# Optimization experiments

Hardware: AMD Instinct MI355X
Metric: run time of the kernel (lower is better)

The kernel has to match this reference:

```python
import jax, jax.numpy as jnp
import numpy as np

NUM_HEADS = 16
D_MODEL = 1024
HEAD_DIM = D_MODEL // NUM_HEADS
SCALE = 8.0 / HEAD_DIM  # use_mup=True
LN_EPS = 1e-5


def setup_inputs() -> dict:
    key = jax.random.key(0)
    ks = jax.random.split(key, 8)
    B, N, M = 2, 2048, 2048
    std = 1.0 / np.sqrt(D_MODEL)
    return {
        "x1": jax.random.normal(ks[0], (B, N, D_MODEL), jnp.float32),
        "x2": jax.random.normal(ks[1], (B, M, D_MODEL), jnp.float32),
        "Wq": jax.random.normal(ks[2], (D_MODEL, D_MODEL), jnp.float32) * std,
        "Wk": jax.random.normal(ks[3], (D_MODEL, D_MODEL), jnp.float32) * std,
        "Wv": jax.random.normal(ks[4], (D_MODEL, D_MODEL), jnp.float32) * std,
        "Wp": jax.random.normal(ks[5], (D_MODEL, D_MODEL), jnp.float32) * std,
        "bp": jnp.zeros((D_MODEL,), jnp.float32),
        "ln_g": jnp.ones((HEAD_DIM,), jnp.float32),
        "ln_b": jnp.zeros((HEAD_DIM,), jnp.float32),
    }


def _layernorm(x, g, b):
    # LayerNorm over last dim (head_dim), eps=1e-5, biased variance (torch default)
    mu = jnp.mean(x, axis=-1, keepdims=True)
    var = jnp.mean(jnp.square(x - mu), axis=-1, keepdims=True)
    return (x - mu) * jax.lax.rsqrt(var + LN_EPS) * g + b


def reference(x1, x2, Wq, Wk, Wv, Wp, bp, ln_g, ln_b):
    B, N, C = x1.shape
    M = x2.shape[1]
    H, D = NUM_HEADS, HEAD_DIM
    # torch Linear: y = x @ W.T  (no qkv bias); reshape to [B, H, L, D]
    q = (x1 @ Wq.T).reshape(B, N, H, D).transpose(0, 2, 1, 3)
    k = (x2 @ Wk.T).reshape(B, M, H, D).transpose(0, 2, 1, 3)
    v = (x2 @ Wv.T).reshape(B, M, H, D).transpose(0, 2, 1, 3)
    # per-head QK LayerNorm (shared params)
    q = _layernorm(q, ln_g, ln_b)
    k = _layernorm(k, ln_g, ln_b)
    q = q * SCALE
    attn = jnp.einsum("bhnd,bhmd->bhnm", q, k)
    attn = jax.nn.softmax(attn, axis=-1)  # causal=False, attn_drop=0
    out = jnp.einsum("bhnm,bhmd->bhnd", attn, v)
    out = out.transpose(0, 2, 1, 3).reshape(B, N, C)
    return out @ Wp.T + bp
```

## Files before the change

### kernel.cpp

```cpp
#include <hip/hip_runtime.h>

#define DEV static __device__ __forceinline__

using bf16x8 = __attribute__((ext_vector_type(8))) short;
using f32x4  = __attribute__((ext_vector_type(4))) float;
using f32x16 = __attribute__((ext_vector_type(16))) float;

#if __has_builtin(__builtin_amdgcn_exp2f)
#define EXP2(x) __builtin_amdgcn_exp2f(x)
#else
#define EXP2(x) exp2f(x)
#endif

DEV unsigned short f2bf(float f) {
  union { float f; unsigned u; } v; v.f = f;
  return (unsigned short)((v.u + 0x7fffu + ((v.u >> 16) & 1u)) >> 16);
}
DEV unsigned pk2(float lo, float hi) {
  return (unsigned)f2bf(lo) | ((unsigned)f2bf(hi) << 16);
}
DEV unsigned cvtpk(float lo, float hi) {
  unsigned r;
  asm("v_cvt_pk_bf16_f32 %0, %1, %2" : "=v"(r) : "v"(lo), "v"(hi));
  return r;
}
DEV void pl32swap(unsigned &a, unsigned &b) {
  asm("v_permlane32_swap_b32 %0, %1" : "+v"(a), "+v"(b));
}
DEV bf16x8 mk8(unsigned a, unsigned b, unsigned c, unsigned d) {
  union { unsigned u[4]; bf16x8 v; } t;
  t.u[0] = a; t.u[1] = b; t.u[2] = c; t.u[3] = d;
  return t.v;
}
DEV f32x4 mfma16(bf16x8 a, bf16x8 b, f32x4 c) {
  return __builtin_amdgcn_mfma_f32_16x16x32_bf16(a, b, c, 0, 0, 0);
}
DEV f32x16 mfma32(bf16x8 a, bf16x8 b, f32x16 c) {
  return __builtin_amdgcn_mfma_f32_32x32x16_bf16(a, b, c, 0, 0, 0);
}
DEV f32x16 zero16() {
  f32x16 z;
#pragma unroll
  for (int i = 0; i < 16; ++i) z[i] = 0.f;
  return z;
}

typedef const __attribute__((address_space(1))) unsigned int* gas1;
typedef __attribute__((address_space(3))) unsigned int* las3;
DEV void gl16(const void* g, void* l) {
  __builtin_amdgcn_global_load_lds((gas1)g, (las3)l, 16, 0, 0);
}

__global__ __launch_bounds__(256, 8)
void conv_bf16(const float* __restrict__ x1, const float* __restrict__ x2,
               const float* __restrict__ Wq, const float* __restrict__ Wk,
               const float* __restrict__ Wv, const float* __restrict__ Wp,
               unsigned short* __restrict__ o)
{
  size_t e = ((size_t)blockIdx.x * 256 + threadIdx.x) * 8;
  const float* s; size_t off;
  if (e < 4194304u)       { s = x1; off = e; }
  else if (e < 8388608u)  { s = x2; off = e - 4194304u; }
  else if (e < 9437184u)  { s = Wq; off = e - 8388608u; }
  else if (e < 10485760u) { s = Wk; off = e - 9437184u; }
  else if (e < 11534336u) { s = Wv; off = e - 10485760u; }
  else                    { s = Wp; off = e - 11534336u; }
  const float4* p = reinterpret_cast<const float4*>(s + off);
  float4 a = p[0], b = p[1];
  int4 r;
  r.x = (int)cvtpk(a.x, a.y); r.y = (int)cvtpk(a.z, a.w);
  r.z = (int)cvtpk(b.x, b.y); r.w = (int)cvtpk(b.z, b.w);
  *reinterpret_cast<int4*>(o + e) = r;
}

__global__ __launch_bounds__(256, 2)
void gemm_qkv_bf(const unsigned short* __restrict__ xb,
                 const float* __restrict__ lg, const float* __restrict__ lb,
                 unsigned short* __restrict__ qb, unsigned short* __restrict__ kb,
                 unsigned short* __restrict__ vtb)
{
  __shared__ short As[128 * 64];
  __shared__ short Bs[128 * 64];
  const int tid = threadIdx.x;
  const int l = tid & 63, w = tid >> 6;
  const int wr = w >> 1, wc = w & 1;
  const int z = blockIdx.z;
  const unsigned short* A = (z == 0) ? xb : (xb + 4194304);
  const unsigned short* W = xb + 8388608 + (size_t)z * 1048576;
  const int id = blockIdx.x + (blockIdx.y << 3);
  const int tl = ((id & 7) << 5) | (id >> 3);
  const int bx = tl & 7, by = tl >> 3;
  const int brow = by * 128, bcol = bx * 128;

  const f32x4 zero = {0.f, 0.f, 0.f, 0.f};
  f32x4 acc[4][4];
#pragma unroll
  for (int mi = 0; mi < 4; ++mi)
#pragma unroll
    for (int ni = 0; ni < 4; ++ni) acc[mi][ni] = zero;

  const int srow = w * 32 + (l >> 3);
  const int scol = (l & 7) * 8;

  for (int kt = 0; kt < 16; ++kt) {
    const unsigned short* ga = A + (size_t)(brow + srow) * 1024 + kt * 64 + scol;
    const unsigned short* gb = W + (size_t)(bcol + srow) * 1024 + kt * 64 + scol;
#pragma unroll
    for (int i = 0; i < 4; ++i) {
      gl16(ga + (size_t)i * 8 * 1024, &As[(w * 32 + i * 8) * 64]);
      gl16(gb + (size_t)i * 8 * 1024, &Bs[(w * 32 + i * 8) * 64]);
    }
    __syncthreads();
#pragma unroll
    for (int kk = 0; kk < 2; ++kk) {
      const int k0 = kk * 32 + ((l >> 4) << 3);
      bf16x8 af[4], bfr[4];
#pragma unroll
      for (int mi = 0; mi < 4; ++mi)
        af[mi] = *reinterpret_cast<const bf16x8*>(
            &As[((wr << 6) + (mi << 4) + (l & 15)) * 64 + k0]);
#pragma unroll
      for (int ni = 0; ni < 4; ++ni)
        bfr[ni] = *reinterpret_cast<const bf16x8*>(
            &Bs[((wc << 6) + (ni << 4) + (l & 15)) * 64 + k0]);
#pragma unroll
      for (int mi = 0; mi < 4; ++mi)
#pragma unroll
        for (int ni = 0; ni < 4; ++ni)
          acc[mi][ni] = mfma16(af[mi], bfr[ni], acc[mi][ni]);
    }
    __syncthreads();
  }

  if (z < 2) {
    unsigned short* dst = (z == 0) ? qb : kb;
    const float scl = (z == 0) ? 0.18033688011112042f : 1.0f;
    const int h = bx * 2 + wc;
    float gw4[4], bw4[4];
#pragma unroll
    for (int ni = 0; ni < 4; ++ni) {
      gw4[ni] = lg[ni * 16 + (l & 15)] * scl;
      bw4[ni] = lb[ni * 16 + (l & 15)] * scl;
    }
#pragma unroll
    for (int mi = 0; mi < 4; ++mi) {
      float ylo[4];
#pragma unroll
      for (int r = 0; r < 4; ++r) {
        float v0 = acc[mi][0][r], v1 = acc[mi][1][r];
        float v2 = acc[mi][2][r], v3 = acc[mi][3][r];
        float s  = (v0 + v1) + (v2 + v3);
        float s2 = (v0 * v0 + v1 * v1) + (v2 * v2 + v3 * v3);
#pragma unroll
        for (int off = 1; off < 16; off <<= 1) {
          s  += __shfl_xor(s, off);
          s2 += __shfl_xor(s2, off);
        }
        float mean = s * (1.f / 64.f);
        float var  = s2 * (1.f / 64.f) - mean * mean;
        float rstd = rsqrtf(var + 1e-5f);
        float y[4];
        y[0] = (v0 - mean) * rstd * gw4[0] + bw4[0];
        y[1] = (v1 - mean) * rstd * gw4[1] + bw4[1];
        y[2] = (v2 - mean) * rstd * gw4[2] + bw4[2];
        y[3] = (v3 - mean) * rstd * gw4[3] + bw4[3];
        if (!(r & 1)) {
          ylo[0] = y[0]; ylo[1] = y[1]; ylo[2] = y[2]; ylo[3] = y[3];
        } else {
          int rowg0 = brow + (wr << 6) + (mi << 4) + ((l >> 4) << 2) + r - 1;
          int b = rowg0 >> 11, n = rowg0 & 2047;
          unsigned short* base =
              dst + (((size_t)(b * 16 + h) << 11) + n) * 64 + (l & 15);
#pragma unroll
          for (int ni = 0; ni < 4; ++ni) {
            unsigned u = cvtpk(ylo[ni], y[ni]);
            base[ni * 16]      = (unsigned short)(u & 0xffffu);
            base[ni * 16 + 64] = (unsigned short)(u >> 16);
          }
        }
      }
    }
  } else {
    const int bb = brow >> 11;
    const int nblk = brow & 2047;
#pragma unroll
    for (int mi = 0; mi < 4; ++mi)
#pragma unroll
      for (int ni = 0; ni < 4; ++ni) {
        int n0 = nblk + (wr << 6) + (mi << 4) + ((l >> 4) << 2);
        int colg = bcol + (wc << 6) + (ni << 4) + (l & 15);
        int h = colg >> 6, d = colg & 63;
        unsigned u0 = cvtpk(acc[mi][ni][0], acc[mi][ni][1]);
        unsigned u1 = cvtpk(acc[mi][ni][2], acc[mi][ni][3]);
        int2 u; u.x = (int)u0; u.y = (int)u1;
        *reinterpret_cast<int2*>(
            &vtb[((size_t)(bb * 16 + h) * 64 + d) * 2048 + n0]) = u;
      }
  }
}

__global__ __launch_bounds__(128)
void attn_fwd(const unsigned short* __restrict__ Q,
              const unsigned short* __restrict__ K,
              const unsigned short* __restrict__ Vt,
              unsigned short* __restrict__ O)
{
  __shared__ short Ks[2][64 * 64];
  __shared__ short Vs[2][64 * 64];
  const int tid = threadIdx.x, w = tid >> 6, l = tid & 63;
  const int lo5 = l & 31, hi = l >> 5;
  const int bh = blockIdx.y;
  const int qbase = blockIdx.x * 64 + w * 32;
  const unsigned short* Qg = Q + ((size_t)bh * 2048 + qbase) * 64;
  const unsigned short* Kg = K + (size_t)bh * 2048 * 64;
  const unsigned short* Vg = Vt + (size_t)bh * 64 * 2048;

  bf16x8 qf[4];
#pragma unroll
  for (int ks = 0; ks < 4; ++ks)
    qf[ks] = *reinterpret_cast<const bf16x8*>(Qg + lo5 * 64 + ks * 16 + hi * 8);

  f32x16 oc0 = zero16(), oc1 = zero16();
  float lsum = 0.f;

  const int srow = tid >> 3;
  const int sc8 = (tid & 7) * 8;
  const int swz = sc8 ^ ((srow & 7) << 3);

  int4 ka0, ka1, ka2, ka3, va0, va1, va2, va3;
  ka0 = *reinterpret_cast<const int4*>(Kg + (srow)      * 64 + sc8);
  ka1 = *reinterpret_cast<const int4*>(Kg + (srow + 16) * 64 + sc8);
  ka2 = *reinterpret_cast<const int4*>(Kg + (srow + 32) * 64 + sc8);
  ka3 = *reinterpret_cast<const int4*>(Kg + (srow + 48) * 64 + sc8);
  va0 = *reinterpret_cast<const int4*>(Vg + (size_t)(srow)      * 2048 + sc8);
  va1 = *reinterpret_cast<const int4*>(Vg + (size_t)(srow + 16) * 2048 + sc8);
  va2 = *reinterpret_cast<const int4*>(Vg + (size_t)(srow + 32) * 2048 + sc8);
  va3 = *reinterpret_cast<const int4*>(Vg + (size_t)(srow + 48) * 2048 + sc8);
  *reinterpret_cast<int4*>(&Ks[0][((srow)      << 6) + swz]) = ka0;
  *reinterpret_cast<int4*>(&Ks[0][((srow + 16) << 6) + swz]) = ka1;
  *reinterpret_cast<int4*>(&Ks[0][((srow + 32) << 6) + swz]) = ka2;
  *reinterpret_cast<int4*>(&Ks[0][((srow + 48) << 6) + swz]) = ka3;
  *reinterpret_cast<int4*>(&Vs[0][((srow)      << 6) + swz]) = va0;
  *reinterpret_cast<int4*>(&Vs[0][((srow + 16) << 6) + swz]) = va1;
  *reinterpret_cast<int4*>(&Vs[0][((srow + 32) << 6) + swz]) = va2;
  *reinterpret_cast<int4*>(&Vs[0][((srow + 48) << 6) + swz]) = va3;
  __syncthreads();

  const unsigned short* kp = Kg + 4096 + srow * 64 + sc8;
  const unsigned short* vp = Vg + 64 + (size_t)srow * 2048 + sc8;

  for (int it = 0; it < 32; ++it) {
    const int cur = it & 1;
    const short* Kc = Ks[cur];
    const short* Vc = Vs[cur];

    if (it < 31) {
      ka0 = *reinterpret_cast<const int4*>(kp);
      ka1 = *reinterpret_cast<const int4*>(kp + 1024);
      ka2 = *reinterpret_cast<const int4*>(kp + 2048);
      ka3 = *reinterpret_cast<const int4*>(kp + 3072);
      va0 = *reinterpret_cast<const int4*>(vp);
      va1 = *reinterpret_cast<const int4*>(vp + 32768);
      va2 = *reinterpret_cast<const int4*>(vp + 65536);
      va3 = *reinterpret_cast<const int4*>(vp + 98304);
      kp += 4096; vp += 64;
    }

    f32x16 s0 = zero16(), s1 = zero16();
    __builtin_amdgcn_s_setprio(1);
#pragma unroll
    for (int ks = 0; ks < 4; ++ks) {
      const int colc = (16 * ks + 8 * hi) ^ ((lo5 & 7) << 3);
      bf16x8 k0 = *reinterpret_cast<const bf16x8*>(&Kc[(lo5 << 6) + colc]);
      s0 = mfma32(k0, qf[ks], s0);
      bf16x8 k1 = *reinterpret_cast<const bf16x8*>(&Kc[((32 + lo5) << 6) + colc]);
      s1 = mfma32(k1, qf[ks], s1);
    }
    __builtin_amdgcn_s_setprio(0);

    auto pvsub = [&](const f32x16& sv, int jbase) {
      float p0[16];
#pragma unroll
      for (int r = 0; r < 16; ++r) p0[r] = EXP2(sv[r]);
      lsum += (((p0[0] + p0[1]) + (p0[2] + p0[3])) +
               ((p0[4] + p0[5]) + (p0[6] + p0[7]))) +
              (((p0[8] + p0[9]) + (p0[10] + p0[11])) +
               ((p0[12] + p0[13]) + (p0[14] + p0[15])));
#pragma unroll
      for (int f = 0; f < 2; ++f) {
        unsigned x  = cvtpk(p0[8 * f + 0], p0[8 * f + 1]);
        unsigned zz = cvtpk(p0[8 * f + 2], p0[8 * f + 3]);
        unsigned y  = cvtpk(p0[8 * f + 4], p0[8 * f + 5]);
        unsigned ww = cvtpk(p0[8 * f + 6], p0[8 * f + 7]);
        pl32swap(x, y);
        pl32swap(zz, ww);
        bf16x8 pa = mk8(x, zz, y, ww);
        const int colc = (jbase + 16 * f + 8 * hi);
        bf16x8 v0 = *reinterpret_cast<const bf16x8*>(
            &Vc[(lo5 << 6) + (colc ^ ((lo5 & 7) << 3))]);
        bf16x8 v1 = *reinterpret_cast<const bf16x8*>(
            &Vc[((32 + lo5) << 6) + (colc ^ ((lo5 & 7) << 3))]);
        __builtin_amdgcn_s_setprio(1);
        oc0 = mfma32(pa, v0, oc0);
        oc1 = mfma32(pa, v1, oc1);
        __builtin_amdgcn_s_setprio(0);
      }
    };
    pvsub(s0, 0);
    pvsub(s1, 32);

    if (it < 31) {
      const int nb = cur ^ 1;
      *reinterpret_cast<int4*>(&Ks[nb][((srow)      << 6) + swz]) = ka0;
      *reinterpret_cast<int4*>(&Ks[nb][((srow + 16) << 6) + swz]) = ka1;
      *reinterpret_cast<int4*>(&Ks[nb][((srow + 32) << 6) + swz]) = ka2;
      *reinterpret_cast<int4*>(&Ks[nb][((srow + 48) << 6) + swz]) = ka3;
      *reinterpret_cast<int4*>(&Vs[nb][((srow)      << 6) + swz]) = va0;
      *reinterpret_cast<int4*>(&Vs[nb][((srow + 16) << 6) + swz]) = va1;
      *reinterpret_cast<int4*>(&Vs[nb][((srow + 32) << 6) + swz]) = va2;
      *reinterpret_cast<int4*>(&Vs[nb][((srow + 48) << 6) + swz]) = va3;
    }
    __syncthreads();
  }

  lsum += __shfl_xor(lsum, 32);
  float inv = 1.f / lsum;
  unsigned short* Og = O + ((size_t)(bh >> 4) * 2048 + qbase) * 1024 + (bh & 15) * 64;
#pragma unroll
  for (int r = 0; r < 16; ++r) {
    int qrow = (r & 3) + 8 * (r >> 2) + 4 * hi;
    float ir = __shfl(inv, qrow);
    Og[qrow * 1024 + lo5]      = f2bf(oc0[r] * ir);
    Og[qrow * 1024 + 32 + lo5] = f2bf(oc1[r] * ir);
  }
}

__global__ __launch_bounds__(256, 2)
void gemm_out_bf(const unsigned short* __restrict__ ob,
                 const unsigned short* __restrict__ wpb,
                 const float* __restrict__ bp, float* __restrict__ out)
{
  __shared__ short As[128 * 64];
  __shared__ short Bs[128 * 64];
  const int tid = threadIdx.x;
  const int l = tid & 63, w = tid >> 6;
  const int wr = w >> 1, wc = w & 1;
  const int id = blockIdx.x + (blockIdx.y << 3);
  const int tl = ((id & 7) << 5) | (id >> 3);
  const int brow = (tl >> 3) * 128, bcol = (tl & 7) * 128;

  const f32x4 zero = {0.f, 0.f, 0.f, 0.f};
  f32x4 acc[4][4];
#pragma unroll
  for (int mi = 0; mi < 4; ++mi)
#pragma unroll
    for (int ni = 0; ni < 4; ++ni) acc[mi][ni] = zero;

  const int srow = w * 32 + (l >> 3);
  const int scol = (l & 7) * 8;

  for (int kt = 0; kt < 16; ++kt) {
    const unsigned short* ga = ob + (size_t)(brow + srow) * 1024 + kt * 64 + scol;
    const unsigned short* gb = wpb + (size_t)(bcol + srow) * 1024 + kt * 64 + scol;
#pragma unroll
    for (int i = 0; i < 4; ++i) {
      gl16(ga + (size_t)i * 8 * 1024, &As[(w * 32 + i * 8) * 64]);
      gl16(gb + (size_t)i * 8 * 1024, &Bs[(w * 32 + i * 8) * 64]);
    }
    __syncthreads();
#pragma unroll
    for (int kk = 0; kk < 2; ++kk) {
      const int k0 = kk * 32 + ((l >> 4) << 3);
      bf16x8 af[4], bfr[4];
#pragma unroll
      for (int mi = 0; mi < 4; ++mi)
        af[mi] = *reinterpret_cast<const bf16x8*>(
            &As[((wr << 6) + (mi << 4) + (l & 15)) * 64 + k0]);
#pragma unroll
      for (int ni = 0; ni < 4; ++ni)
        bfr[ni] = *reinterpret_cast<const bf16x8*>(
            &Bs[((wc << 6) + (ni << 4) + (l & 15)) * 64 + k0]);
#pragma unroll
      for (int mi = 0; mi < 4; ++mi)
#pragma unroll
        for (int ni = 0; ni < 4; ++ni)
          acc[mi][ni] = mfma16(af[mi], bfr[ni], acc[mi][ni]);
    }
    __syncthreads();
  }

  float bias[4];
#pragma unroll
  for (int ni = 0; ni < 4; ++ni)
    bias[ni] = bp[bcol + (wc << 6) + (ni << 4) + (l & 15)];
#pragma unroll
  for (int mi = 0; mi < 4; ++mi)
#pragma unroll
    for (int ni = 0; ni < 4; ++ni)
#pragma unroll
      for (int r = 0; r < 4; ++r) {
        int rowg = brow + (wr << 6) + (mi << 4) + ((l >> 4) << 2) + r;
        int colg = bcol + (wc << 6) + (ni << 4) + (l & 15);
        out[(size_t)rowg * 1024 + colg] = acc[mi][ni][r] + bias[ni];
      }
}

extern "C" void kernel_launch(void* const* d_in, const int* in_sizes, int n_in,
                              void* d_out, int out_size, void* d_ws, size_t ws_size,
                              hipStream_t stream)
{
  const float* x1 = (const float*)d_in[0];
  const float* x2 = (const float*)d_in[1];
  const float* Wq = (const float*)d_in[2];
  const float* Wk = (const float*)d_in[3];
  const float* Wv = (const float*)d_in[4];
  const float* Wp = (const float*)d_in[5];
  const float* bp = (const float*)d_in[6];
  const float* lg = (const float*)d_in[7];
  const float* lb = (const float*)d_in[8];

  char* wsb = (char*)d_ws;
  unsigned short* xb   = (unsigned short*)wsb;
  unsigned short* qb   = (unsigned short*)(wsb + 25165824);
  unsigned short* kb   = qb + 4194304;
  unsigned short* vtb  = kb + 4194304;
  unsigned short* obuf = vtb + 4194304;
  float* out = (float*)d_out;

  conv_bf16<<<6144, 256, 0, stream>>>(x1, x2, Wq, Wk, Wv, Wp, xb);
  gemm_qkv_bf<<<dim3(8, 32, 3), 256, 0, stream>>>(xb, lg, lb, qb, kb, vtb);
  attn_fwd<<<dim3(32, 32), 128, 0, stream>>>(qb, kb, vtb, obuf);
  gemm_out_bf<<<dim3(8, 32), 256, 0, stream>>>(obuf,
      xb + 11534336, bp, out);
}
```

Baseline: 130.3 us.

## Split attention over key range into two halves and combine partials

Splits the attention kernel's key loop into two halves via a third grid dimension, doubling the number of blocks. Each half writes unnormalized bf16 partial outputs and row sums to workspace, and a new combine kernel adds them and normalizes. The row-sum accumulation moves from scalar adds to an extra MFMA against a ones vector. This aims to improve occupancy and load balance on the GPU, at the cost of an extra launch, extra global traffic, and bf16 rounding of the partials.

Result: slower. 143.1 us (+9.8%).

```diff
diff --git a/kernel.cpp b/kernel.cpp
--- a/kernel.cpp
+++ b/kernel.cpp
@@ -16,8 +16,9 @@
   union { float f; unsigned u; } v; v.f = f;
   return (unsigned short)((v.u + 0x7fffu + ((v.u >> 16) & 1u)) >> 16);
 }
-DEV unsigned pk2(float lo, float hi) {
-  return (unsigned)f2bf(lo) | ((unsigned)f2bf(hi) << 16);
+DEV float bf2f(unsigned short b) {
+  union { unsigned u; float f; } v; v.u = ((unsigned)b) << 16;
+  return v.f;
 }
 DEV unsigned cvtpk(float lo, float hi) {
   unsigned r;
@@ -203,13 +204,16 @@
 void attn_fwd(const unsigned short* __restrict__ Q,
               const unsigned short* __restrict__ K,
               const unsigned short* __restrict__ Vt,
-              unsigned short* __restrict__ O)
+              unsigned short* __restrict__ pnum,
+              float* __restrict__ plsum)
 {
   __shared__ short Ks[2][64 * 64];
   __shared__ short Vs[2][64 * 64];
   const int tid = threadIdx.x, w = tid >> 6, l = tid & 63;
   const int lo5 = l & 31, hi = l >> 5;
   const int bh = blockIdx.y;
+  const int half = blockIdx.z;
+  const int tbase = half * 16;
   const int qbase = blockIdx.x * 64 + w * 32;
   const unsigned short* Qg = Q + ((size_t)bh * 2048 + qbase) * 64;
   const unsigned short* Kg = K + (size_t)bh * 2048 * 64;
@@ -219,23 +223,27 @@
 #pragma unroll
   for (int ks = 0; ks < 4; ++ks)
     qf[ks] = *reinterpret_cast<const bf16x8*>(Qg + lo5 * 64 + ks * 16 + hi * 8);
-
-  f32x16 oc0 = zero16(), oc1 = zero16();
-  float lsum = 0.f;
+  const bf16x8 ones = mk8(0x3F803F80u, 0x3F803F80u, 0x3F803F80u, 0x3F803F80u);
+
+  f32x16 oc0 = zero16(), oc1 = zero16(), ls = zero16();
 
   const int srow = tid >> 3;
   const int sc8 = (tid & 7) * 8;
   const int swz = sc8 ^ ((srow & 7) << 3);
 
   int4 ka0, ka1, ka2, ka3, va0, va1, va2, va3;
-  ka0 = *reinterpret_cast<const int4*>(Kg + (srow)      * 64 + sc8);
-  ka1 = *reinterpret_cast<const int4*>(Kg + (srow + 16) * 64 + sc8);
-  ka2 = *reinterpret_cast<const int4*>(Kg + (srow + 32) * 64 + sc8);
-  ka3 = *reinterpret_cast<const int4*>(Kg + (srow + 48) * 64 + sc8);
-  va0 = *reinterpret_cast<const int4*>(Vg + (size_t)(srow)      * 2048 + sc8);
-  va1 = *reinterpret_cast<const int4*>(Vg + (size_t)(srow + 16) * 2048 + sc8);
-  va2 = *reinterpret_cast<const int4*>(Vg + (size_t)(srow + 32) * 2048 + sc8);
-  va3 = *reinterpret_cast<const int4*>(Vg + (size_t)(srow + 48) * 2048 + sc8);
+  {
+    const unsigned short* k0g = Kg + tbase * 4096;
+    const unsigned short* v0g = Vg + tbase * 64;
+    ka0 = *reinterpret_cast<const int4*>(k0g + (srow)      * 64 + sc8);
+    ka1 = *reinterpret_cast<const int4*>(k0g + (srow + 16) * 64 + sc8);
+    ka2 = *reinterpret_cast<const int4*>(k0g + (srow + 32) * 64 + sc8);
+    ka3 = *reinterpret_cast<const int4*>(k0g + (srow + 48) * 64 + sc8);
+    va0 = *reinterpret_cast<const int4*>(v0g + (size_t)(srow)      * 2048 + sc8);
+    va1 = *reinterpret_cast<const int4*>(v0g + (size_t)(srow + 16) * 2048 + sc8);
+    va2 = *reinterpret_cast<const int4*>(v0g + (size_t)(srow + 32) * 2048 + sc8);
+    va3 = *reinterpret_cast<const int4*>(v0g + (size_t)(srow + 48) * 2048 + sc8);
+  }
   *reinterpret_cast<int4*>(&Ks[0][((srow)      << 6) + swz]) = ka0;
   *reinterpret_cast<int4*>(&Ks[0][((srow + 16) << 6) + swz]) = ka1;
   *reinterpret_cast<int4*>(&Ks[0][((srow + 32) << 6) + swz]) = ka2;
@@ -246,15 +254,15 @@
   *reinterpret_cast<int4*>(&Vs[0][((srow + 48) << 6) + swz]) = va3;
   __syncthreads();
 
-  const unsigned short* kp = Kg + 4096 + srow * 64 + sc8;
-  const unsigned short* vp = Vg + 64 + (size_t)srow * 2048 + sc8;
-
-  for (int it = 0; it < 32; ++it) {
+  const unsigned short* kp = Kg + (tbase + 1) * 4096 + srow * 64 + sc8;
+  const unsigned short* vp = Vg + (tbase + 1) * 64 + (size_t)srow * 2048 + sc8;
+
+  for (int it = 0; it < 16; ++it) {
     const int cur = it & 1;
     const short* Kc = Ks[cur];
     const short* Vc = Vs[cur];
 
-    if (it < 31) {
+    if (it < 15) {
       ka0 = *reinterpret_cast<const int4*>(kp);
       ka1 = *reinterpret_cast<const int4*>(kp + 1024);
       ka2 = *reinterpret_cast<const int4*>(kp + 2048);
@@ -282,10 +290,6 @@
       float p0[16];
 #pragma unroll
       for (int r = 0; r < 16; ++r) p0[r] = EXP2(sv[r]);
-      lsum += (((p0[0] + p0[1]) + (p0[2] + p0[3])) +
-               ((p0[4] + p0[5]) + (p0[6] + p0[7]))) +
-              (((p0[8] + p0[9]) + (p0[10] + p0[11])) +
-               ((p0[12] + p0[13]) + (p0[14] + p0[15])));
 #pragma unroll
       for (int f = 0; f < 2; ++f) {
         unsigned x  = cvtpk(p0[8 * f + 0], p0[8 * f + 1]);
@@ -303,13 +307,14 @@
         __builtin_amdgcn_s_setprio(1);
         oc0 = mfma32(pa, v0, oc0);
         oc1 = mfma32(pa, v1, oc1);
+        ls  = mfma32(pa, ones, ls);
         __builtin_amdgcn_s_setprio(0);
       }
     };
     pvsub(s0, 0);
     pvsub(s1, 32);
 
-    if (it < 31) {
+    if (it < 15) {
       const int nb = cur ^ 1;
       *reinterpret_cast<int4*>(&Ks[nb][((srow)      << 6) + swz]) = ka0;
       *reinterpret_cast<int4*>(&Ks[nb][((srow + 16) << 6) + swz]) = ka1;
@@ -323,16 +328,51 @@
     __syncthreads();
   }
 
-  lsum += __shfl_xor(lsum, 32);
-  float inv = 1.f / lsum;
-  unsigned short* Og = O + ((size_t)(bh >> 4) * 2048 + qbase) * 1024 + (bh & 15) * 64;
+  unsigned short* Pn = pnum + ((size_t)(half * 32 + bh) * 2048 + qbase) * 64;
 #pragma unroll
   for (int r = 0; r < 16; ++r) {
     int qrow = (r & 3) + 8 * (r >> 2) + 4 * hi;
-    float ir = __shfl(inv, qrow);
-    Og[qrow * 1024 + lo5]      = f2bf(oc0[r] * ir);
-    Og[qrow * 1024 + 32 + lo5] = f2bf(oc1[r] * ir);
-  }
+    Pn[qrow * 64 + lo5]      = f2bf(oc0[r]);
+    Pn[qrow * 64 + 32 + lo5] = f2bf(oc1[r]);
+  }
+  if (lo5 == 0) {
+    float* Pl = plsum + (size_t)(half * 32 + bh) * 2048 + qbase;
+#pragma unroll
+    for (int r = 0; r < 16; ++r)
+      Pl[(r & 3) + 8 * (r >> 2) + 4 * hi] = ls[r];
+  }
+}
+
+__global__ __launch_bounds__(256, 8)
+void attn_combine(const unsigned short* __restrict__ pnum,
+                  const float* __restrict__ plsum,
+                  unsigned short* __restrict__ obuf)
+{
+  const int t = blockIdx.x * 256 + threadIdx.x;
+  const int bh = t >> 14;
+  const int rem = t & 16383;
+  const int q = rem >> 3, dblk = rem & 7;
+  const size_t i0 = (((size_t)bh * 2048) + q) * 64 + dblk * 8;
+  const size_t i1 = i0 + (size_t)32 * 2048 * 64;
+  ushort4 a0 = *reinterpret_cast<const ushort4*>(pnum + i0);
+  ushort4 a1 = *reinterpret_cast<const ushort4*>(pnum + i0 + 4);
+  ushort4 b0 = *reinterpret_cast<const ushort4*>(pnum + i1);
+  ushort4 b1 = *reinterpret_cast<const ushort4*>(pnum + i1 + 4);
+  float ls = plsum[bh * 2048 + q] + plsum[65536 + bh * 2048 + q];
+  float inv = 1.f / ls;
+  ushort4 o0, o1;
+  o0.x = f2bf((bf2f(a0.x) + bf2f(b0.x)) * inv);
+  o0.y = f2bf((bf2f(a0.y) + bf2f(b0.y)) * inv);
+  o0.z = f2bf((bf2f(a0.z) + bf2f(b0.z)) * inv);
+  o0.w = f2bf((bf2f(a0.w) + bf2f(b0.w)) * inv);
+  o1.x = f2bf((bf2f(a1.x) + bf2f(b1.x)) * inv);
+  o1.y = f2bf((bf2f(a1.y) + bf2f(b1.y)) * inv);
+  o1.z = f2bf((bf2f(a1.z) + bf2f(b1.z)) * inv);
+  o1.w = f2bf((bf2f(a1.w) + bf2f(b1.w)) * inv);
+  unsigned short* dst = obuf + ((size_t)(bh >> 4) * 2048 + q) * 1024 +
+                        (bh & 15) * 64 + dblk * 8;
+  *reinterpret_cast<ushort4*>(dst) = o0;
+  *reinterpret_cast<ushort4*>(dst + 4) = o1;
 }
 
 __global__ __launch_bounds__(256, 2)
@@ -425,11 +465,14 @@
   unsigned short* kb   = qb + 4194304;
   unsigned short* vtb  = kb + 4194304;
   unsigned short* obuf = vtb + 4194304;
+  unsigned short* pnum = obuf + 4194304;
+  float* plsum = (float*)(wsb + 75497472);
   float* out = (float*)d_out;
 
   conv_bf16<<<6144, 256, 0, stream>>>(x1, x2, Wq, Wk, Wv, Wp, xb);
   gemm_qkv_bf<<<dim3(8, 32, 3), 256, 0, stream>>>(xb, lg, lb, qb, kb, vtb);
-  attn_fwd<<<dim3(32, 32), 128, 0, stream>>>(qb, kb, vtb, obuf);
+  attn_fwd<<<dim3(32, 32, 2), 128, 0, stream>>>(qb, kb, vtb, pnum, plsum);
+  attn_combine<<<2048, 256, 0, stream>>>(pnum, plsum, obuf);
   gemm_out_bf<<<dim3(8, 32), 256, 0, stream>>>(obuf,
       xb + 11534336, bp, out);
 }
```
